# Optimization experiments

Hardware: AMD Instinct MI355X
Metric: run time of the kernel (lower is better)

The kernel has to match this reference:

```python
import jax, jax.numpy as jnp
import numpy as np
import math

D_MODEL = 64
N_HEADS = 4
D_HEAD = D_MODEL // N_HEADS
SCALE = math.sqrt(D_HEAD)
B, NQ, NK = 32, 16384, 31


def setup_inputs() -> dict:
    key = jax.random.key(0)
    kq, kk, kv, km, kw, kb = jax.random.split(key, 6)
    Q = jax.random.normal(kq, (B, NQ, D_MODEL), dtype=jnp.float32)
    K = jax.random.normal(kk, (B, NK, D_MODEL), dtype=jnp.float32)
    V = jax.random.normal(kv, (B, NK, D_MODEL), dtype=jnp.float32)
    mask = jax.random.randint(km, (B, NK), 0, 2).astype(jnp.bool_)
    # out_proj: nn.Linear(d_model, d_model)
    lim = 1.0 / math.sqrt(D_MODEL)
    W_out = jax.random.uniform(kw, (D_MODEL, D_MODEL), minval=-lim, maxval=lim, dtype=jnp.float32)
    b_out = jax.random.uniform(kb, (D_MODEL,), minval=-lim, maxval=lim, dtype=jnp.float32)
    return {"Q": Q, "K": K, "V": V, "mask": mask, "W_out": W_out, "b_out": b_out}


def reference(Q, K, V, mask, W_out, b_out):
    Bn, Nq, D = Q.shape
    Nk = K.shape[1]
    # (B, H, N, d_head)
    q = Q.reshape(Bn, Nq, N_HEADS, D_HEAD).transpose(0, 2, 1, 3)
    k = K.reshape(Bn, Nk, N_HEADS, D_HEAD).transpose(0, 2, 1, 3)
    v = V.reshape(Bn, Nk, N_HEADS, D_HEAD).transpose(0, 2, 1, 3)
    # (B, H, Nq, Nk)
    attn = jnp.einsum('bhqd,bhkd->bhqk', q, k) / SCALE
    attn = jnp.where(mask[:, None, None, :], attn, -jnp.inf)
    attn = jax.nn.softmax(attn, axis=-1)
    attn = jnp.nan_to_num(attn, nan=0.0)
    out = jnp.einsum('bhqk,bhkd->bhqd', attn, v)
    out = out.transpose(0, 2, 1, 3).reshape(Bn, Nq, D)
    return out @ W_out.T + b_out
```

## Files before the change

kernel.cpp:

```cpp
#include <hip/hip_runtime.h>
#include <math.h>

typedef _Float16 half4_t __attribute__((ext_vector_type(4)));
typedef __fp16   fp16x2  __attribute__((ext_vector_type(2)));
typedef float    f32x4   __attribute__((ext_vector_type(4)));

#define B_   32
#define NQ_  16384
#define NK_  31
#define DM_  64

static __device__ __forceinline__ half4_t cvt4(f32x4 f) {
  fp16x2 lo = __builtin_amdgcn_cvt_pkrtz(f[0], f[1]);
  fp16x2 hi = __builtin_amdgcn_cvt_pkrtz(f[2], f[3]);
  half4_t r;
  r[0] = (_Float16)lo[0]; r[1] = (_Float16)lo[1];
  r[2] = (_Float16)hi[0]; r[3] = (_Float16)hi[1];
  return r;
}

__global__ __launch_bounds__(256) void attn(
    const float* __restrict__ Q, const float* __restrict__ K,
    const float* __restrict__ V, const unsigned char* __restrict__ mraw,
    const float* __restrict__ W, const float* __restrict__ bout,
    float* __restrict__ out) {
  int b    = blockIdx.x >> 5;
  int blk  = blockIdx.x & 31;
  int tid  = threadIdx.x;
  int wave = tid >> 6, lane = tid & 63;
  int lq = lane & 15, quad = lane >> 4;

  unsigned mb;
  {
    unsigned char c0 = 0, c1 = 0;
    if (lane < 62) { c0 = mraw[2 * lane]; c1 = mraw[2 * lane + 1]; }
    unsigned long long m3f =
        __ballot(lane < 62 && (c0 == 0x3f || c1 == 0x3f));
    unsigned long long moff =
        __ballot(lane < 62 && ((((2 * lane) & 3) != 0 && c0 != 0) || c1 != 0));
    int mode = m3f ? 2 : (moff ? 0 : 1);
    int nz = 0;
    if (lane < NK_) {
      int idx = b * NK_ + lane;
      nz = (mode == 0) ? (mraw[idx] != 0)
         : (mode == 1) ? (((const int*)mraw)[idx] != 0)
                       : (((const float*)mraw)[idx] != 0.0f);
    }
    mb = (unsigned)__ballot(nz) & 0x7fffffffu;
  }

  f32x4 cbias[2];
  #pragma unroll
  for (int tt = 0; tt < 2; ++tt)
    #pragma unroll
    for (int r = 0; r < 4; ++r) {
      int key = 16 * tt + 4 * quad + r;
      cbias[tt][r] = ((mb >> key) & 1u) ? 0.0f : -1e30f;
    }

  const f32x4 fzero = {0.f, 0.f, 0.f, 0.f};

  half4_t kf[2][4];
  #pragma unroll
  for (int tt = 0; tt < 2; ++tt) {
    int k = 16 * tt + lq;
    #pragma unroll
    for (int h = 0; h < 4; ++h) {
      f32x4 f = fzero;
      if (k < NK_)
        f = *(const f32x4*)(K + ((size_t)b * NK_ + k) * DM_ + 16 * h + 4 * quad);
      kf[tt][h] = cvt4(f * 0.25f);
    }
  }

  half4_t vwf[4][8];
  {
    half4_t af[8];
    #pragma unroll
    for (int s = 0; s < 8; ++s) {
      int k = 16 * (s & 1) + lq, h = s >> 1;
      f32x4 f = fzero;
      if (k < NK_)
        f = *(const f32x4*)(V + ((size_t)b * NK_ + k) * DM_ + 16 * h + 4 * quad);
      af[s] = cvt4(f);
    }
    half4_t bf[4][4];
    #pragma unroll
    for (int dt = 0; dt < 4; ++dt)
      #pragma unroll
      for (int h = 0; h < 4; ++h) {
        f32x4 f = *(const f32x4*)(W + (16 * dt + lq) * DM_ + 16 * h + 4 * quad);
        bf[dt][h] = cvt4(f);
      }
    #pragma unroll
    for (int dt = 0; dt < 4; ++dt)
      #pragma unroll
      for (int s = 0; s < 8; ++s) {
        f32x4 m = __builtin_amdgcn_mfma_f32_16x16x16f16(af[s], bf[dt][s >> 1],
                                                        fzero, 0, 0, 0);
        vwf[dt][s] = cvt4(m);
      }
  }

  f32x4 bias[4];
  #pragma unroll
  for (int dt = 0; dt < 4; ++dt)
    bias[dt] = *(const f32x4*)(bout + 16 * dt + 4 * quad);

  int w = blk * 4 + wave;
  const float* qrow = Q + ((size_t)b * NQ_ + lq) * DM_ + 4 * quad;

  f32x4 qraw[4];
  #pragma unroll
  for (int h = 0; h < 4; ++h)
    qraw[h] = *(const f32x4*)(qrow + (size_t)(w * 16) * DM_ + 16 * h);

  #pragma unroll 1
  for (int it = 0; it < 8; ++it) {
    int q0 = (w + it * 128) * 16;

    f32x4 qnext[4];
    if (it < 7) {
      #pragma unroll
      for (int h = 0; h < 4; ++h)
        qnext[h] = *(const f32x4*)(qrow + (size_t)(q0 + 2048) * DM_ + 16 * h);
    }

    half4_t qf[4];
    #pragma unroll
    for (int h = 0; h < 4; ++h) qf[h] = cvt4(qraw[h]);

    half4_t pf[8];
    #pragma unroll
    for (int h = 0; h < 4; ++h) {
      f32x4 c0 = __builtin_amdgcn_mfma_f32_16x16x16f16(kf[0][h], qf[h], cbias[0], 0, 0, 0);
      f32x4 c1 = __builtin_amdgcn_mfma_f32_16x16x16f16(kf[1][h], qf[h], cbias[1], 0, 0, 0);
      f32x4 e0, e1;
      #pragma unroll
      for (int r = 0; r < 4; ++r) { e0[r] = __expf(c0[r]); e1[r] = __expf(c1[r]); }
      float sum = (e0[0] + e0[1]) + (e0[2] + e0[3]) +
                  (e1[0] + e1[1]) + (e1[2] + e1[3]);
      sum += __shfl_xor(sum, 16);
      sum += __shfl_xor(sum, 32);
      float inv = (sum > 0.f) ? __builtin_amdgcn_rcpf(sum) : 0.f;
      pf[2 * h + 0] = cvt4(e0 * inv);
      pf[2 * h + 1] = cvt4(e1 * inv);
    }

    f32x4 acc[4] = {fzero, fzero, fzero, fzero};
    #pragma unroll
    for (int s = 0; s < 8; ++s)
      #pragma unroll
      for (int dt = 0; dt < 4; ++dt)
        acc[dt] = __builtin_amdgcn_mfma_f32_16x16x16f16(vwf[dt][s], pf[s], acc[dt], 0, 0, 0);

    float* obase = out + ((size_t)b * NQ_ + q0 + lq) * DM_ + 4 * quad;
    #pragma unroll
    for (int dt = 0; dt < 4; ++dt)
      *(f32x4*)(obase + 16 * dt) = acc[dt] + bias[dt];

    if (it < 7) {
      #pragma unroll
      for (int h = 0; h < 4; ++h) qraw[h] = qnext[h];
    }
  }
}

extern "C" void kernel_launch(void* const* d_in, const int* in_sizes, int n_in,
                              void* d_out, int out_size, void* d_ws, size_t ws_size,
                              hipStream_t stream) {
  const float*         Q    = (const float*)d_in[0];
  const float*         K    = (const float*)d_in[1];
  const float*         V    = (const float*)d_in[2];
  const unsigned char* mask = (const unsigned char*)d_in[3];
  const float*         W    = (const float*)d_in[4];
  const float*         bo   = (const float*)d_in[5];
  float*               out  = (float*)d_out;

  hipLaunchKernelGGL(attn, dim3(B_ * 32), dim3(256), 0, stream,
                     Q, K, V, mask, W, bo, out);
}
```

Baseline: 256.6 us.

## Stage V·W product in shared memory, split precompute across waves, double grid

Each wave now computes one quarter of the fused V·W_out fp16 matrix and writes it to LDS, replacing the per-wave 32-register copy. Waves read it from LDS inside the main loop. The grid is doubled, with fewer Q tiles per block, and launch bounds request 4 blocks per CU to raise occupancy. Output stores become nontemporal. The trade-off is extra LDS reads per MFMA, a block barrier, and more blocks that each repeat the mask, K and precompute setup.

```diff
diff --git a/kernel.cpp b/kernel.cpp
--- a/kernel.cpp
+++ b/kernel.cpp
@@ -9,6 +9,7 @@
 #define NQ_  16384
 #define NK_  31
 #define DM_  64
+#define PITCH 132
 
 static __device__ __forceinline__ half4_t cvt4(f32x4 f) {
   fp16x2 lo = __builtin_amdgcn_cvt_pkrtz(f[0], f[1]);
@@ -19,13 +20,15 @@
   return r;
 }
 
-__global__ __launch_bounds__(256) void attn(
+__global__ __launch_bounds__(256, 4) void attn(
     const float* __restrict__ Q, const float* __restrict__ K,
     const float* __restrict__ V, const unsigned char* __restrict__ mraw,
     const float* __restrict__ W, const float* __restrict__ bout,
     float* __restrict__ out) {
-  int b    = blockIdx.x >> 5;
-  int blk  = blockIdx.x & 31;
+  __shared__ _Float16 vw[64 * PITCH];
+
+  int b    = blockIdx.x >> 6;
+  int blk  = blockIdx.x & 63;
   int tid  = threadIdx.x;
   int wave = tid >> 6, lane = tid & 63;
   int lq = lane & 15, quad = lane >> 4;
@@ -73,39 +76,31 @@
     }
   }
 
-  half4_t vwf[4][8];
   {
-    half4_t af[8];
+    int dt = wave;
+    half4_t bf[4];
+    #pragma unroll
+    for (int h = 0; h < 4; ++h) {
+      f32x4 f = *(const f32x4*)(W + (16 * dt + lq) * DM_ + 16 * h + 4 * quad);
+      bf[h] = cvt4(f);
+    }
     #pragma unroll
     for (int s = 0; s < 8; ++s) {
       int k = 16 * (s & 1) + lq, h = s >> 1;
       f32x4 f = fzero;
       if (k < NK_)
         f = *(const f32x4*)(V + ((size_t)b * NK_ + k) * DM_ + 16 * h + 4 * quad);
-      af[s] = cvt4(f);
+      f32x4 m = __builtin_amdgcn_mfma_f32_16x16x16f16(cvt4(f), bf[h], fzero, 0, 0, 0);
+      *(half4_t*)&vw[(16 * dt + lq) * PITCH + 16 * s + 4 * quad] = cvt4(m);
     }
-    half4_t bf[4][4];
-    #pragma unroll
-    for (int dt = 0; dt < 4; ++dt)
-      #pragma unroll
-      for (int h = 0; h < 4; ++h) {
-        f32x4 f = *(const f32x4*)(W + (16 * dt + lq) * DM_ + 16 * h + 4 * quad);
-        bf[dt][h] = cvt4(f);
-      }
-    #pragma unroll
-    for (int dt = 0; dt < 4; ++dt)
-      #pragma unroll
-      for (int s = 0; s < 8; ++s) {
-        f32x4 m = __builtin_amdgcn_mfma_f32_16x16x16f16(af[s], bf[dt][s >> 1],
-                                                        fzero, 0, 0, 0);
-        vwf[dt][s] = cvt4(m);
-      }
   }
 
   f32x4 bias[4];
   #pragma unroll
   for (int dt = 0; dt < 4; ++dt)
     bias[dt] = *(const f32x4*)(bout + 16 * dt + 4 * quad);
+
+  __syncthreads();
 
   int w = blk * 4 + wave;
   const float* qrow = Q + ((size_t)b * NQ_ + lq) * DM_ + 4 * quad;
@@ -116,14 +111,14 @@
     qraw[h] = *(const f32x4*)(qrow + (size_t)(w * 16) * DM_ + 16 * h);
 
   #pragma unroll 1
-  for (int it = 0; it < 8; ++it) {
-    int q0 = (w + it * 128) * 16;
+  for (int it = 0; it < 4; ++it) {
+    int q0 = (w + it * 256) * 16;
 
     f32x4 qnext[4];
-    if (it < 7) {
+    if (it < 3) {
       #pragma unroll
       for (int h = 0; h < 4; ++h)
-        qnext[h] = *(const f32x4*)(qrow + (size_t)(q0 + 2048) * DM_ + 16 * h);
+        qnext[h] = *(const f32x4*)(qrow + (size_t)(q0 + 4096) * DM_ + 16 * h);
     }
 
     half4_t qf[4];
@@ -151,15 +146,19 @@
     #pragma unroll
     for (int s = 0; s < 8; ++s)
       #pragma unroll
-      for (int dt = 0; dt < 4; ++dt)
-        acc[dt] = __builtin_amdgcn_mfma_f32_16x16x16f16(vwf[dt][s], pf[s], acc[dt], 0, 0, 0);
+      for (int dt = 0; dt < 4; ++dt) {
+        half4_t a = *(const half4_t*)&vw[(16 * dt + lq) * PITCH + 16 * s + 4 * quad];
+        acc[dt] = __builtin_amdgcn_mfma_f32_16x16x16f16(a, pf[s], acc[dt], 0, 0, 0);
+      }
 
     float* obase = out + ((size_t)b * NQ_ + q0 + lq) * DM_ + 4 * quad;
     #pragma unroll
-    for (int dt = 0; dt < 4; ++dt)
-      *(f32x4*)(obase + 16 * dt) = acc[dt] + bias[dt];
+    for (int dt = 0; dt < 4; ++dt) {
+      f32x4 r = acc[dt] + bias[dt];
+      __builtin_nontemporal_store(r, (f32x4*)(obase + 16 * dt));
+    }
 
-    if (it < 7) {
+    if (it < 3) {
       #pragma unroll
       for (int h = 0; h < 4; ++h) qraw[h] = qnext[h];
     }
@@ -177,6 +176,6 @@
   const float*         bo   = (const float*)d_in[5];
   float*               out  = (float*)d_out;
 
-  hipLaunchKernelGGL(attn, dim3(B_ * 32), dim3(256), 0, stream,
+  hipLaunchKernelGGL(attn, dim3(B_ * 64), dim3(256), 0, stream,
                      Q, K, V, mask, W, bo, out);
 }
```

Result: slower. 352.8 us (+37.5%).
